# Kernel optimization log

Hardware: AMD Instinct MI355X
Metric: run time of the kernel (lower is better)

The kernel has to match this reference:

```python
import jax, jax.numpy as jnp
import numpy as np

BN_EPS = 1e-5


def _gin_layer(x, src, dst, n_nodes, W1, b1, W2, b2, gamma, beta):
    # GINConv with eps=0: z_i = x_i + sum_{(j->i) in E} x_j, then 2-layer MLP
    agg = jax.ops.segment_sum(x[src], dst, num_segments=n_nodes)  # [N, d]
    z = x + agg
    z = jax.nn.relu(z @ W1 + b1) @ W2 + b2
    # BatchNorm1d (training mode: biased batch statistics over node dim)
    mean = jnp.mean(z, axis=0)
    var = jnp.var(z, axis=0)
    z = (z - mean) * jax.lax.rsqrt(var + BN_EPS) * gamma + beta
    return jax.nn.relu(z)  # dropout p=0 -> identity


def setup_inputs() -> dict:
    key = jax.random.key(0)
    ks = jax.random.split(key, 8)
    N, E, D, L = 50000, 800000, 128, 2
    h = jax.random.normal(ks[0], (N, D), dtype=jnp.float32)
    edge_index = jax.random.randint(ks[1], (2, E), 0, N, dtype=jnp.int64)
    scale = 1.0 / np.sqrt(D)
    W1 = jax.random.normal(ks[2], (L, D, D), dtype=jnp.float32) * scale
    b1 = jax.random.normal(ks[3], (L, D), dtype=jnp.float32) * 0.01
    W2 = jax.random.normal(ks[4], (L, D, D), dtype=jnp.float32) * scale
    b2 = jax.random.normal(ks[5], (L, D), dtype=jnp.float32) * 0.01
    gamma = jnp.ones((L, D), dtype=jnp.float32)
    beta = jnp.zeros((L, D), dtype=jnp.float32)
    return {"h": h, "edge_index": edge_index, "W1": W1, "b1": b1,
            "W2": W2, "b2": b2, "gamma": gamma, "beta": beta}


def reference(h, edge_index, W1, b1, W2, b2, gamma, beta):
    src, dst = edge_index[0], edge_index[1]
    n_nodes = h.shape[0]
    n_layers = W1.shape[0]
    outs = []
    x = h
    for i in range(n_layers):
        x = _gin_layer(x, src, dst, n_nodes, W1[i], b1[i], W2[i], b2[i], gamma[i], beta[i])
        outs.append(x)
    return jnp.stack(outs)  # [L, N, D] == hs[1:]
```

## Files before the change

kernel.cpp:

```cpp
#include <hip/hip_runtime.h>

#define D 128
#define BN_EPS 1e-5f

typedef __attribute__((ext_vector_type(8))) short short8;
typedef __attribute__((ext_vector_type(4))) float f32x4;

__device__ inline unsigned short f2bf(float f) {
    union { float f; unsigned int u; } v; v.f = f;
    unsigned int u = v.u;
    unsigned int r = (u + 0x7FFFu + ((u >> 16) & 1u)) >> 16;
    return (unsigned short)r;
}

__device__ inline float bfbits2f(unsigned int bits) {
    union { unsigned int u; float f; } v; v.u = bits;
    return v.f;
}

__device__ inline float4 bf2f4(uint2 v) {
    float4 r;
    r.x = bfbits2f(v.x << 16);
    r.y = bfbits2f(v.x & 0xFFFF0000u);
    r.z = bfbits2f(v.y << 16);
    r.w = bfbits2f(v.y & 0xFFFF0000u);
    return r;
}

__global__ void hist_rank(const int* __restrict__ dst, int* __restrict__ cnt,
                          int* __restrict__ rank, int E) {
    int e = blockIdx.x * blockDim.x + threadIdx.x;
    if (e >= E) return;
    rank[e] = atomicAdd(&cnt[dst[e]], 1);
}

__global__ void reduce_cnt(const int* __restrict__ cnt, int* __restrict__ bsum, int n) {
    __shared__ int s[256];
    int tid = threadIdx.x;
    int i = blockIdx.x * 256 + tid;
    s[tid] = (i < n) ? cnt[i] : 0;
    __syncthreads();
    for (int ofs = 128; ofs > 0; ofs >>= 1) {
        if (tid < ofs) s[tid] += s[tid + ofs];
        __syncthreads();
    }
    if (tid == 0) bsum[blockIdx.x] = s[0];
}

__global__ void scan_bsums(const int* __restrict__ bsum, int* __restrict__ blockOff,
                           int* __restrict__ offN, int nb) {
    __shared__ int s[256];
    int tid = threadIdx.x;
    int v = (tid < nb) ? bsum[tid] : 0;
    s[tid] = v;
    __syncthreads();
    for (int ofs = 1; ofs < 256; ofs <<= 1) {
        int t = (tid >= ofs) ? s[tid - ofs] : 0;
        __syncthreads();
        s[tid] += t;
        __syncthreads();
    }
    if (tid < nb) blockOff[tid] = s[tid] - v;
    if (tid == nb - 1) *offN = s[tid];
}

__global__ void scan_partial(const int* __restrict__ cnt, int* __restrict__ off,
                             const int* __restrict__ blockOff, int n) {
    __shared__ int s[256];
    int tid = threadIdx.x;
    int i = blockIdx.x * 256 + tid;
    int v = (i < n) ? cnt[i] : 0;
    s[tid] = v;
    __syncthreads();
    for (int ofs = 1; ofs < 256; ofs <<= 1) {
        int t = (tid >= ofs) ? s[tid - ofs] : 0;
        __syncthreads();
        s[tid] += t;
        __syncthreads();
    }
    if (i < n) off[i] = blockOff[blockIdx.x] + s[tid] - v;
}

__global__ void fill2(const int* __restrict__ src, const int* __restrict__ dst,
                      const int* __restrict__ rank, const int* __restrict__ off,
                      int* __restrict__ eidx, int E) {
    int e = blockIdx.x * blockDim.x + threadIdx.x;
    if (e >= E) return;
    eidx[off[dst[e]] + rank[e]] = src[e];
}

__global__ void wprep(const float* __restrict__ W1, const float* __restrict__ W2,
                      unsigned short* __restrict__ Wt, int L) {
    int idx = blockIdx.x * 256 + threadIdx.x;
    int m = idx >> 14;
    int rem = idx & 16383;
    int c = rem >> 7, k = rem & 127;
    const float* W = (m < L) ? (W1 + (size_t)m * D * D) : (W2 + (size_t)(m - L) * D * D);
    Wt[(size_t)m * D * D + c * D + k] = f2bf(W[k * D + c]);
}

__global__ void x2bf(const float* __restrict__ x, unsigned short* __restrict__ xb, int n8) {
    int i = blockIdx.x * 256 + threadIdx.x;
    if (i >= n8) return;
    float4 a = reinterpret_cast<const float4*>(x)[2 * i];
    float4 b = reinterpret_cast<const float4*>(x)[2 * i + 1];
    uint4 o;
    o.x = (unsigned)f2bf(a.x) | ((unsigned)f2bf(a.y) << 16);
    o.y = (unsigned)f2bf(a.z) | ((unsigned)f2bf(a.w) << 16);
    o.z = (unsigned)f2bf(b.x) | ((unsigned)f2bf(b.y) << 16);
    o.w = (unsigned)f2bf(b.z) | ((unsigned)f2bf(b.w) << 16);
    reinterpret_cast<uint4*>(xb)[i] = o;
}

__global__ __launch_bounds__(256) void gather_bf(
        const unsigned short* __restrict__ xb, const int* __restrict__ off,
        const int* __restrict__ eidx, unsigned short* __restrict__ zb, int N) {
    int t = blockIdx.x * blockDim.x + threadIdx.x;
    int node = t >> 5;
    if (node >= N) return;
    int lane = t & 31;
    int beg = off[node], end = off[node + 1];
    float4 acc = bf2f4(*reinterpret_cast<const uint2*>(xb + (size_t)node * D + lane * 4));
    int e = beg;
    for (; e + 2 <= end; e += 2) {
        int s0 = eidx[e], s1 = eidx[e + 1];
        uint2 v0 = *reinterpret_cast<const uint2*>(xb + (size_t)s0 * D + lane * 4);
        uint2 v1 = *reinterpret_cast<const uint2*>(xb + (size_t)s1 * D + lane * 4);
        float4 f0 = bf2f4(v0), f1 = bf2f4(v1);
        acc.x += f0.x + f1.x; acc.y += f0.y + f1.y;
        acc.z += f0.z + f1.z; acc.w += f0.w + f1.w;
    }
    if (e < end) {
        int s0 = eidx[e];
        float4 f0 = bf2f4(*reinterpret_cast<const uint2*>(xb + (size_t)s0 * D + lane * 4));
        acc.x += f0.x; acc.y += f0.y; acc.z += f0.z; acc.w += f0.w;
    }
    uint2 o;
    o.x = (unsigned)f2bf(acc.x) | ((unsigned)f2bf(acc.y) << 16);
    o.y = (unsigned)f2bf(acc.z) | ((unsigned)f2bf(acc.w) << 16);
    *reinterpret_cast<uint2*>(zb + (size_t)node * D + lane * 4) = o;
}

__global__ __launch_bounds__(256) void gemm1_mfma(
        const unsigned short* __restrict__ A, const unsigned short* __restrict__ Wt,
        const float* __restrict__ bias, unsigned short* __restrict__ Out, int N) {
    const int tid = threadIdx.x;
    const int lane = tid & 63, wv = tid >> 6;
    const int r0 = blockIdx.x * 128 + wv * 32;
    const int koff = (lane >> 4) << 3;
    const int col = lane & 15;

    int ar0 = r0 + col;       if (ar0 >= N) ar0 = N - 1;
    int ar1 = r0 + 16 + col;  if (ar1 >= N) ar1 = N - 1;
    const unsigned short* ap0 = A + (size_t)ar0 * D + koff;
    const unsigned short* ap1 = A + (size_t)ar1 * D + koff;
    const unsigned short* wp  = Wt + (size_t)col * D + koff;

    f32x4 acc[2][8];
    #pragma unroll
    for (int ct = 0; ct < 8; ct++) {
        float b = bias[ct * 16 + col];
        acc[0][ct] = (f32x4){b, b, b, b};
        acc[1][ct] = (f32x4){b, b, b, b};
    }
    #pragma unroll
    for (int ks = 0; ks < 4; ks++) {
        short8 a0 = *reinterpret_cast<const short8*>(ap0 + ks * 32);
        short8 a1 = *reinterpret_cast<const short8*>(ap1 + ks * 32);
        #pragma unroll
        for (int ct = 0; ct < 8; ct++) {
            short8 bfr = *reinterpret_cast<const short8*>(wp + (size_t)ct * 16 * D + ks * 32);
            acc[0][ct] = __builtin_amdgcn_mfma_f32_16x16x32_bf16(a0, bfr, acc[0][ct], 0, 0, 0);
            acc[1][ct] = __builtin_amdgcn_mfma_f32_16x16x32_bf16(a1, bfr, acc[1][ct], 0, 0, 0);
        }
    }
    #pragma unroll
    for (int t = 0; t < 2; t++) {
        #pragma unroll
        for (int ct = 0; ct < 8; ct++) {
            #pragma unroll
            for (int r = 0; r < 4; r++) {
                int row = r0 + t * 16 + ((lane >> 4) << 2) + r;
                if (row < N)
                    Out[(size_t)row * D + ct * 16 + col] = f2bf(fmaxf(acc[t][ct][r], 0.f));
            }
        }
    }
}

__global__ __launch_bounds__(256) void gemm2_mfma(
        const unsigned short* __restrict__ A, const unsigned short* __restrict__ Wt,
        const float* __restrict__ bias, float* __restrict__ Out,
        float* __restrict__ gstats, int N) {
    __shared__ float sStat[2 * D];
    const int tid = threadIdx.x;
    if (tid < 2 * D) sStat[tid] = 0.f;
    __syncthreads();

    const int lane = tid & 63, wv = tid >> 6;
    const int r0 = blockIdx.x * 128 + wv * 32;
    const int koff = (lane >> 4) << 3;
    const int col = lane & 15;

    int ar0 = r0 + col;       if (ar0 >= N) ar0 = N - 1;
    int ar1 = r0 + 16 + col;  if (ar1 >= N) ar1 = N - 1;
    const unsigned short* ap0 = A + (size_t)ar0 * D + koff;
    const unsigned short* ap1 = A + (size_t)ar1 * D + koff;
    const unsigned short* wp  = Wt + (size_t)col * D + koff;

    f32x4 acc[2][8];
    #pragma unroll
    for (int ct = 0; ct < 8; ct++) {
        float b = bias[ct * 16 + col];
        acc[0][ct] = (f32x4){b, b, b, b};
        acc[1][ct] = (f32x4){b, b, b, b};
    }
    #pragma unroll
    for (int ks = 0; ks < 4; ks++) {
        short8 a0 = *reinterpret_cast<const short8*>(ap0 + ks * 32);
        short8 a1 = *reinterpret_cast<const short8*>(ap1 + ks * 32);
        #pragma unroll
        for (int ct = 0; ct < 8; ct++) {
            short8 bfr = *reinterpret_cast<const short8*>(wp + (size_t)ct * 16 * D + ks * 32);
            acc[0][ct] = __builtin_amdgcn_mfma_f32_16x16x32_bf16(a0, bfr, acc[0][ct], 0, 0, 0);
            acc[1][ct] = __builtin_amdgcn_mfma_f32_16x16x32_bf16(a1, bfr, acc[1][ct], 0, 0, 0);
        }
    }
    #pragma unroll
    for (int ct = 0; ct < 8; ct++) {
        float s = 0.f, q = 0.f;
        #pragma unroll
        for (int t = 0; t < 2; t++) {
            #pragma unroll
            for (int r = 0; r < 4; r++) {
                int row = r0 + t * 16 + ((lane >> 4) << 2) + r;
                float v = acc[t][ct][r];
                if (row < N) {
                    Out[(size_t)row * D + ct * 16 + col] = v;
                    s += v; q += v * v;
                }
            }
        }
        s += __shfl_xor(s, 16); q += __shfl_xor(q, 16);
        s += __shfl_xor(s, 32); q += __shfl_xor(q, 32);
        if (lane < 16) {
            atomicAdd(&sStat[ct * 16 + lane], s);
            atomicAdd(&sStat[D + ct * 16 + lane], q);
        }
    }
    __syncthreads();
    if (tid < 2 * D) atomicAdd(&gstats[tid], sStat[tid]);
}

__global__ void bn_relu_bf(float* __restrict__ y, unsigned short* __restrict__ xb,
                           const float* __restrict__ stats,
                           const float* __restrict__ gamma, const float* __restrict__ beta,
                           int N) {
    int i = blockIdx.x * blockDim.x + threadIdx.x;
    int n4 = N * D / 4;
    if (i >= n4) return;
    int c0 = (i << 2) & (D - 1);
    float4 v = reinterpret_cast<float4*>(y)[i];
    float o[4] = {v.x, v.y, v.z, v.w};
    float invN = 1.0f / (float)N;
    #pragma unroll
    for (int j = 0; j < 4; j++) {
        int c = c0 + j;
        float mean = stats[c] * invN;
        float var  = stats[D + c] * invN - mean * mean;
        float sc = rsqrtf(var + BN_EPS) * gamma[c];
        float t = (o[j] - mean) * sc + beta[c];
        o[j] = fmaxf(t, 0.f);
    }
    float4 r; r.x = o[0]; r.y = o[1]; r.z = o[2]; r.w = o[3];
    reinterpret_cast<float4*>(y)[i] = r;
    uint2 ob;
    ob.x = (unsigned)f2bf(o[0]) | ((unsigned)f2bf(o[1]) << 16);
    ob.y = (unsigned)f2bf(o[2]) | ((unsigned)f2bf(o[3]) << 16);
    reinterpret_cast<uint2*>(xb)[i] = ob;
}

extern "C" void kernel_launch(void* const* d_in, const int* in_sizes, int n_in,
                              void* d_out, int out_size, void* d_ws, size_t ws_size,
                              hipStream_t stream) {
    const float* h     = (const float*)d_in[0];
    const int*   ei    = (const int*)d_in[1];
    const float* W1    = (const float*)d_in[2];
    const float* b1    = (const float*)d_in[3];
    const float* W2    = (const float*)d_in[4];
    const float* b2    = (const float*)d_in[5];
    const float* gamma = (const float*)d_in[6];
    const float* beta  = (const float*)d_in[7];
    float* out = (float*)d_out;

    const int N = in_sizes[0] / D;
    const int E = in_sizes[1] / 2;
    const int L = in_sizes[2] / (D * D);
    const int nb = (N + 255) / 256;

    unsigned short* zb  = (unsigned short*)d_ws;
    unsigned short* xb  = zb + (size_t)N * D;
    unsigned short* Wt  = xb + (size_t)N * D;
    float* stats = (float*)(Wt + (size_t)2 * L * D * D);
    int* cnt      = (int*)(stats + (size_t)L * 2 * D);
    int* off      = cnt + N;
    int* bsum     = off + N + 1;
    int* blockOff = bsum + nb;
    int* rank     = blockOff + nb;
    int* eidx     = rank + E;

    const int* src = ei;
    const int* dst = ei + E;

    const int n4 = N * D / 4;
    const int n8 = N * D / 8;
    const int ewBlocks = (E + 255) / 256;
    const int gatherBlocks = (N * 32 + 255) / 256;
    const int gemmBlocks = (N + 127) / 128;
    const int bnBlocks = (n4 + 255) / 256;
    const int wprepBlocks = (2 * L * D * D) / 256;

    hipMemsetAsync(cnt, 0, N * sizeof(int), stream);
    hipMemsetAsync(stats, 0, (size_t)L * 2 * D * sizeof(float), stream);
    wprep<<<wprepBlocks, 256, 0, stream>>>(W1, W2, Wt, L);
    x2bf<<<(n8 + 255) / 256, 256, 0, stream>>>(h, xb, n8);

    hist_rank<<<ewBlocks, 256, 0, stream>>>(dst, cnt, rank, E);
    reduce_cnt<<<nb, 256, 0, stream>>>(cnt, bsum, N);
    scan_bsums<<<1, 256, 0, stream>>>(bsum, blockOff, off + N, nb);
    scan_partial<<<nb, 256, 0, stream>>>(cnt, off, blockOff, N);
    fill2<<<ewBlocks, 256, 0, stream>>>(src, dst, rank, off, eidx, E);

    for (int l = 0; l < L; l++) {
        float* y = out + (size_t)l * N * D;

        gather_bf<<<gatherBlocks, 256, 0, stream>>>(xb, off, eidx, zb, N);
        gemm1_mfma<<<gemmBlocks, 256, 0, stream>>>(zb, Wt + (size_t)l * D * D,
                                                   b1 + (size_t)l * D, zb, N);
        gemm2_mfma<<<gemmBlocks, 256, 0, stream>>>(zb, Wt + (size_t)(L + l) * D * D,
                                                   b2 + (size_t)l * D, y, stats + (size_t)l * 2 * D, N);
        bn_relu_bf<<<bnBlocks, 256, 0, stream>>>(y, xb, stats + (size_t)l * 2 * D,
                                                 gamma + (size_t)l * D, beta + (size_t)l * D, N);
    }
}
```

Measured before the change: 244.2 us.

## Split gather into column slices and store edge indices as 16-bit

```diff
diff --git a/kernel.cpp b/kernel.cpp
--- a/kernel.cpp
+++ b/kernel.cpp
@@ -81,12 +81,13 @@
     if (i < n) off[i] = blockOff[blockIdx.x] + s[tid] - v;
 }
 
+template<typename IdxT>
 __global__ void fill2(const int* __restrict__ src, const int* __restrict__ dst,
                       const int* __restrict__ rank, const int* __restrict__ off,
-                      int* __restrict__ eidx, int E) {
+                      IdxT* __restrict__ eidx, int E) {
     int e = blockIdx.x * blockDim.x + threadIdx.x;
     if (e >= E) return;
-    eidx[off[dst[e]] + rank[e]] = src[e];
+    eidx[off[dst[e]] + rank[e]] = (IdxT)src[e];
 }
 
 __global__ void wprep(const float* __restrict__ W1, const float* __restrict__ W2,
@@ -112,33 +113,37 @@
     reinterpret_cast<uint4*>(xb)[i] = o;
 }
 
-__global__ __launch_bounds__(256) void gather_bf(
+template<typename IdxT>
+__global__ __launch_bounds__(256) void gather_bf4(
         const unsigned short* __restrict__ xb, const int* __restrict__ off,
-        const int* __restrict__ eidx, unsigned short* __restrict__ zb, int N) {
-    int t = blockIdx.x * blockDim.x + threadIdx.x;
-    int node = t >> 5;
+        const IdxT* __restrict__ eidx, unsigned short* __restrict__ zb, int N) {
+    const int slice = blockIdx.x & 3;
+    const int node = (blockIdx.x >> 2) * 32 + (threadIdx.x >> 3);
     if (node >= N) return;
-    int lane = t & 31;
+    const int lane8 = threadIdx.x & 7;
+    const int colOfs = slice * 32 + lane8 * 4;
+    const unsigned short* base = xb + colOfs;
+
+    float4 acc = bf2f4(*reinterpret_cast<const uint2*>(base + (size_t)node * D));
     int beg = off[node], end = off[node + 1];
-    float4 acc = bf2f4(*reinterpret_cast<const uint2*>(xb + (size_t)node * D + lane * 4));
     int e = beg;
     for (; e + 2 <= end; e += 2) {
-        int s0 = eidx[e], s1 = eidx[e + 1];
-        uint2 v0 = *reinterpret_cast<const uint2*>(xb + (size_t)s0 * D + lane * 4);
-        uint2 v1 = *reinterpret_cast<const uint2*>(xb + (size_t)s1 * D + lane * 4);
+        int s0 = (int)eidx[e], s1 = (int)eidx[e + 1];
+        uint2 v0 = *reinterpret_cast<const uint2*>(base + (size_t)s0 * D);
+        uint2 v1 = *reinterpret_cast<const uint2*>(base + (size_t)s1 * D);
         float4 f0 = bf2f4(v0), f1 = bf2f4(v1);
         acc.x += f0.x + f1.x; acc.y += f0.y + f1.y;
         acc.z += f0.z + f1.z; acc.w += f0.w + f1.w;
     }
     if (e < end) {
-        int s0 = eidx[e];
-        float4 f0 = bf2f4(*reinterpret_cast<const uint2*>(xb + (size_t)s0 * D + lane * 4));
+        int s0 = (int)eidx[e];
+        float4 f0 = bf2f4(*reinterpret_cast<const uint2*>(base + (size_t)s0 * D));
         acc.x += f0.x; acc.y += f0.y; acc.z += f0.z; acc.w += f0.w;
     }
     uint2 o;
     o.x = (unsigned)f2bf(acc.x) | ((unsigned)f2bf(acc.y) << 16);
     o.y = (unsigned)f2bf(acc.z) | ((unsigned)f2bf(acc.w) << 16);
-    *reinterpret_cast<uint2*>(zb + (size_t)node * D + lane * 4) = o;
+    *reinterpret_cast<uint2*>(zb + (size_t)node * D + colOfs) = o;
 }
 
 __global__ __launch_bounds__(256) void gemm1_mfma(
@@ -307,7 +312,7 @@
     int* bsum     = off + N + 1;
     int* blockOff = bsum + nb;
     int* rank     = blockOff + nb;
-    int* eidx     = rank + E;
+    void* eidx    = (void*)(rank + E);
 
     const int* src = ei;
     const int* dst = ei + E;
@@ -315,10 +320,11 @@
     const int n4 = N * D / 4;
     const int n8 = N * D / 8;
     const int ewBlocks = (E + 255) / 256;
-    const int gatherBlocks = (N * 32 + 255) / 256;
+    const int gatherBlocks = 4 * ((N + 31) / 32);
     const int gemmBlocks = (N + 127) / 128;
     const int bnBlocks = (n4 + 255) / 256;
     const int wprepBlocks = (2 * L * D * D) / 256;
+    const bool small = (N <= 65535);
 
     hipMemsetAsync(cnt, 0, N * sizeof(int), stream);
     hipMemsetAsync(stats, 0, (size_t)L * 2 * D * sizeof(float), stream);
@@ -329,12 +335,21 @@
     reduce_cnt<<<nb, 256, 0, stream>>>(cnt, bsum, N);
     scan_bsums<<<1, 256, 0, stream>>>(bsum, blockOff, off + N, nb);
     scan_partial<<<nb, 256, 0, stream>>>(cnt, off, blockOff, N);
-    fill2<<<ewBlocks, 256, 0, stream>>>(src, dst, rank, off, eidx, E);
+    if (small)
+        fill2<unsigned short><<<ewBlocks, 256, 0, stream>>>(src, dst, rank, off,
+                                                            (unsigned short*)eidx, E);
+    else
+        fill2<int><<<ewBlocks, 256, 0, stream>>>(src, dst, rank, off, (int*)eidx, E);
 
     for (int l = 0; l < L; l++) {
         float* y = out + (size_t)l * N * D;
 
-        gather_bf<<<gatherBlocks, 256, 0, stream>>>(xb, off, eidx, zb, N);
+        if (small)
+            gather_bf4<unsigned short><<<gatherBlocks, 256, 0, stream>>>(
+                xb, off, (const unsigned short*)eidx, zb, N);
+        else
+            gather_bf4<int><<<gatherBlocks, 256, 0, stream>>>(
+                xb, off, (const int*)eidx, zb, N);
         gemm1_mfma<<<gemmBlocks, 256, 0, stream>>>(zb, Wt + (size_t)l * D * D,
                                                    b1 + (size_t)l * D, zb, N);
         gemm2_mfma<<<gemmBlocks, 256, 0, stream>>>(zb, Wt + (size_t)(L + l) * D * D,
```

Measured after the change: 261.3 us. 1.07x slower.
